# Kernel tuning notes

Measured on AMD Instinct MI355X. Metric: run time of the kernel, lower is better.

The kernel has to match this reference:

```python
import jax, jax.numpy as jnp
import numpy as np

HEADS = 4
DIM_HEAD = 64


def setup_inputs() -> dict:
    key = jax.random.key(0)
    k1, k2, k3, k4 = jax.random.split(key, 4)
    dim = 256
    hidden = HEADS * DIM_HEAD  # 256
    x = jax.random.normal(k1, (16, dim, 64, 64), dtype=jnp.float32)
    # 1x1 conv weights stored as [out_c, in_c]
    w_qkv = jax.random.normal(k2, (3 * hidden, dim), dtype=jnp.float32) * (1.0 / np.sqrt(dim))
    w_out = jax.random.normal(k3, (dim, hidden), dtype=jnp.float32) * (1.0 / np.sqrt(hidden))
    b_out = jax.random.normal(k4, (dim,), dtype=jnp.float32) * 0.01
    gamma = jnp.ones((dim,), dtype=jnp.float32) * 1e-05
    return {"x": x, "w_qkv": w_qkv, "w_out": w_out, "b_out": b_out, "gamma": gamma}


def reference(x, w_qkv, w_out, b_out, gamma):
    b, c, h, w = x.shape
    n = h * w
    # 1x1 conv == channel matmul
    qkv = jnp.einsum('oc,bchw->bohw', w_qkv, x)  # [b, 3*heads*dh, h, w]
    qkv = qkv.reshape(b, 3, HEADS, DIM_HEAD, n)  # channel split order: (qkv, heads, c)
    q, k, v = qkv[:, 0], qkv[:, 1], qkv[:, 2]    # each [b, heads, dh, n]
    k = jax.nn.softmax(k, axis=-1)               # softmax over spatial tokens
    context = jnp.einsum('bhdn,bhen->bhde', k, v)  # [b, heads, dh, dh]
    out = jnp.einsum('bhde,bhdn->bhen', context, q)  # [b, heads, dh, n]
    out = out.reshape(b, HEADS * DIM_HEAD, h, w)
    y = jnp.einsum('oc,bchw->bohw', w_out, out) + b_out[None, :, None, None]
    return y * gamma[None, :, None, None] + x
```

## Files before the change

### kernel.cpp

```cpp
#include <hip/hip_runtime.h>
#include <stdint.h>

typedef short s16x8 __attribute__((ext_vector_type(8)));
typedef float f32x4 __attribute__((ext_vector_type(4)));

__device__ __forceinline__ float bits2f(unsigned short u) {
    union { unsigned int i; float f; } c; c.i = ((unsigned int)u) << 16; return c.f;
}
__device__ __forceinline__ unsigned short f2bits(float f) {
    union { float f; unsigned int i; } c; c.f = f;
    unsigned int x = c.i;
    unsigned int r = (x + 0x7FFFu + ((x >> 16) & 1u)) >> 16;
    return (unsigned short)r;
}
__device__ __forceinline__ unsigned int pack2(float a, float b) {
    return (unsigned int)f2bits(a) | ((unsigned int)f2bits(b) << 16);
}

__global__ __launch_bounds__(256) void k_cvt(
    const float* __restrict__ src, unsigned short* __restrict__ dst, int n8)
{
    int i = blockIdx.x * 256 + threadIdx.x;
    if (i >= n8) return;
    const float* s = src + (size_t)i * 8;
    float4 a = *(const float4*)s, b = *(const float4*)(s + 4);
    unsigned int q[4] = { pack2(a.x, a.y), pack2(a.z, a.w), pack2(b.x, b.y), pack2(b.z, b.w) };
    *(s16x8*)(dst + (size_t)i * 8) = *(s16x8*)q;
}

__global__ __launch_bounds__(256) void k_transpose(
    const unsigned short* __restrict__ src, unsigned short* __restrict__ dst,
    int RS, int DS)
{
    int dr = blockIdx.x * 256 + threadIdx.x;
    int c0 = blockIdx.y * 8;
    __align__(16) unsigned short tmp[8];
#pragma unroll
    for (int j = 0; j < 8; ++j) tmp[j] = src[(size_t)(c0 + j) * RS + dr];
    *(s16x8*)(dst + (size_t)dr * DS + c0) = *(s16x8*)tmp;
}

template <int BF32>
__global__ __launch_bounds__(256) void gemm_bt(
    const unsigned short* __restrict__ A, const void* __restrict__ Bt,
    unsigned short* __restrict__ C,
    int K, int Kstep, int lda, int ldb, int ldc,
    long Abs, long Bbs, long Cbs)
{
    __shared__ unsigned short As[128][72];
    __shared__ unsigned short Bs[128][72];
    int bz = blockIdx.z;
    int b = bz & 15, kc = bz >> 4;
    int m0 = blockIdx.y * 128, n0 = blockIdx.x * 128;
    const unsigned short* Ab = A + (size_t)b * Abs + (size_t)m0 * lda + (size_t)kc * Kstep;
    size_t boff = (size_t)b * Bbs + (size_t)n0 * ldb + (size_t)kc * Kstep;
    int t = threadIdx.x;
    int w = t >> 6, l = t & 63, lm = l & 15, lq = l >> 4;
    int mw = (w >> 1) * 64, nw = (w & 1) * 64;

    f32x4 acc[4][4];
    f32x4 zero = {0.f, 0.f, 0.f, 0.f};
#pragma unroll
    for (int i = 0; i < 4; ++i)
#pragma unroll
        for (int j = 0; j < 4; ++j) acc[i][j] = zero;

    for (int kk = 0; kk < K; kk += 64) {
#pragma unroll
        for (int i = 0; i < 4; ++i) {
            int idx = t + i * 256;
            int r = idx >> 3, ch = idx & 7;
            *(s16x8*)&As[r][ch * 8] = *(const s16x8*)(Ab + (size_t)r * lda + kk + ch * 8);
            if (BF32) {
                const float* bp = (const float*)Bt + boff + (size_t)r * ldb + kk + ch * 8;
                float4 v0 = *(const float4*)bp, v1 = *(const float4*)(bp + 4);
                unsigned int q[4] = { pack2(v0.x, v0.y), pack2(v0.z, v0.w),
                                      pack2(v1.x, v1.y), pack2(v1.z, v1.w) };
                *(s16x8*)&Bs[r][ch * 8] = *(s16x8*)q;
            } else {
                const unsigned short* bp = (const unsigned short*)Bt + boff + (size_t)r * ldb + kk + ch * 8;
                *(s16x8*)&Bs[r][ch * 8] = *(const s16x8*)bp;
            }
        }
        __syncthreads();
#pragma unroll
        for (int ks = 0; ks < 2; ++ks) {
            s16x8 af[4], bfr[4];
#pragma unroll
            for (int mi = 0; mi < 4; ++mi) af[mi]  = *(const s16x8*)&As[mw + mi * 16 + lm][ks * 32 + lq * 8];
#pragma unroll
            for (int ni = 0; ni < 4; ++ni) bfr[ni] = *(const s16x8*)&Bs[nw + ni * 16 + lm][ks * 32 + lq * 8];
#pragma unroll
            for (int mi = 0; mi < 4; ++mi)
#pragma unroll
                for (int ni = 0; ni < 4; ++ni)
                    acc[mi][ni] = __builtin_amdgcn_mfma_f32_16x16x32_bf16(af[mi], bfr[ni], acc[mi][ni], 0, 0, 0);
        }
        __syncthreads();
    }

    unsigned short* Cb = C + (size_t)bz * Cbs;
#pragma unroll
    for (int mi = 0; mi < 4; ++mi)
#pragma unroll
        for (int r = 0; r < 4; ++r) {
            int m = m0 + mw + mi * 16 + lq * 4 + r;
#pragma unroll
            for (int ni = 0; ni < 4; ++ni) {
                int n = n0 + nw + ni * 16 + lm;
                Cb[(size_t)m * ldc + n] = f2bits(acc[mi][ni][r]);
            }
        }
}

template <int EPI>
__global__ __launch_bounds__(256) void gemm_bn(
    const unsigned short* __restrict__ A, const float* __restrict__ B,
    void* __restrict__ C,
    int K, int lda, int ldb, int ldc,
    long Abs, long Bbs, long Cbs,
    const float* __restrict__ Xres,
    const float* __restrict__ gamma,
    const float* __restrict__ bias)
{
    __shared__ unsigned short As[128][72];
    __shared__ unsigned short Bs[64][130];
    int bz = blockIdx.z;
    int m0 = blockIdx.y * 128, n0 = blockIdx.x * 128;
    const unsigned short* Ab = A + (size_t)bz * Abs + (size_t)m0 * lda;
    const float* Bb = B + (size_t)bz * Bbs + n0;
    int t = threadIdx.x;
    int w = t >> 6, l = t & 63, lm = l & 15, lq = l >> 4;
    int mw = (w >> 1) * 64, nw = (w & 1) * 64;

    f32x4 acc[4][4];
    f32x4 zero = {0.f, 0.f, 0.f, 0.f};
#pragma unroll
    for (int i = 0; i < 4; ++i)
#pragma unroll
        for (int j = 0; j < 4; ++j) acc[i][j] = zero;

    for (int kk = 0; kk < K; kk += 64) {
#pragma unroll
        for (int i = 0; i < 4; ++i) {
            int idx = t + i * 256;
            int r = idx >> 3, ch = idx & 7;
            *(s16x8*)&As[r][ch * 8] = *(const s16x8*)(Ab + (size_t)r * lda + kk + ch * 8);
        }
#pragma unroll
        for (int i = 0; i < 4; ++i) {
            int idx = t + i * 256;
            int c = idx >> 4, cc = idx & 15;
            const float* bp = Bb + (size_t)(kk + c) * ldb + cc * 8;
            float4 v0 = *(const float4*)bp, v1 = *(const float4*)(bp + 4);
            unsigned int* q = (unsigned int*)&Bs[c][cc * 8];
            q[0] = pack2(v0.x, v0.y); q[1] = pack2(v0.z, v0.w);
            q[2] = pack2(v1.x, v1.y); q[3] = pack2(v1.z, v1.w);
        }
        __syncthreads();
#pragma unroll
        for (int ks = 0; ks < 2; ++ks) {
            s16x8 af[4];
#pragma unroll
            for (int mi = 0; mi < 4; ++mi) af[mi] = *(const s16x8*)&As[mw + mi * 16 + lm][ks * 32 + lq * 8];
#pragma unroll
            for (int ni = 0; ni < 4; ++ni) {
                s16x8 bfr;
#pragma unroll
                for (int j = 0; j < 8; ++j) bfr[j] = (short)Bs[ks * 32 + lq * 8 + j][nw + ni * 16 + lm];
#pragma unroll
                for (int mi = 0; mi < 4; ++mi)
                    acc[mi][ni] = __builtin_amdgcn_mfma_f32_16x16x32_bf16(af[mi], bfr, acc[mi][ni], 0, 0, 0);
            }
        }
        __syncthreads();
    }

#pragma unroll
    for (int mi = 0; mi < 4; ++mi)
#pragma unroll
        for (int r = 0; r < 4; ++r) {
            int m = m0 + mw + mi * 16 + lq * 4 + r;
            float g = 0.f, bo = 0.f;
            if (EPI == 1) { g = gamma[m]; bo = bias[m]; }
#pragma unroll
            for (int ni = 0; ni < 4; ++ni) {
                int n = n0 + nw + ni * 16 + lm;
                size_t idx = (size_t)m * ldc + n;
                float v = acc[mi][ni][r];
                if (EPI == 1) {
                    float* Cb = (float*)C + (size_t)bz * Cbs;
                    Cb[idx] = g * (v + bo) + Xres[(size_t)bz * Cbs + idx];
                } else {
                    unsigned short* Cb = (unsigned short*)C + (size_t)bz * Cbs;
                    Cb[idx] = f2bits(v);
                }
            }
        }
}

__global__ __launch_bounds__(256) void k_softmax(unsigned short* __restrict__ kbuf)
{
    unsigned short* p = kbuf + (size_t)blockIdx.x * 4096;
    int t = threadIdx.x;
    __shared__ float red[4];

    s16x8 r0 = *(const s16x8*)(p + t * 16);
    s16x8 r1 = *(const s16x8*)(p + t * 16 + 8);
    float v[16];
    float m = -1e30f;
#pragma unroll
    for (int i = 0; i < 8; ++i) { v[i] = bits2f((unsigned short)r0[i]); v[8 + i] = bits2f((unsigned short)r1[i]); }
#pragma unroll
    for (int i = 0; i < 16; ++i) m = fmaxf(m, v[i]);
#pragma unroll
    for (int off = 32; off >= 1; off >>= 1) m = fmaxf(m, __shfl_xor(m, off));
    if ((t & 63) == 0) red[t >> 6] = m;
    __syncthreads();
    m = fmaxf(fmaxf(red[0], red[1]), fmaxf(red[2], red[3]));
    __syncthreads();

    float s = 0.f;
#pragma unroll
    for (int i = 0; i < 16; ++i) { v[i] = __expf(v[i] - m); s += v[i]; }
#pragma unroll
    for (int off = 32; off >= 1; off >>= 1) s += __shfl_xor(s, off);
    if ((t & 63) == 0) red[t >> 6] = s;
    __syncthreads();
    s = red[0] + red[1] + red[2] + red[3];
    float inv = 1.0f / s;

    __align__(16) unsigned short otmp[16];
#pragma unroll
    for (int i = 0; i < 16; ++i) otmp[i] = f2bits(v[i] * inv);
    *(s16x8*)(p + t * 16) = *(s16x8*)(otmp);
    *(s16x8*)(p + t * 16 + 8) = *(s16x8*)(otmp + 8);
}

__global__ __launch_bounds__(256) void k_gred(
    const unsigned short* __restrict__ Gp, unsigned short* __restrict__ G)
{
    int gid = blockIdx.x * 256 + threadIdx.x;
    int b = gid >> 13;
    size_t i8 = (size_t)(gid & 8191) * 8;
    float s[8] = {0.f, 0.f, 0.f, 0.f, 0.f, 0.f, 0.f, 0.f};
#pragma unroll
    for (int kc = 0; kc < 8; ++kc) {
        s16x8 v = *(const s16x8*)(Gp + (size_t)(kc * 16 + b) * 65536 + i8);
#pragma unroll
        for (int j = 0; j < 8; ++j) s[j] += bits2f((unsigned short)v[j]);
    }
    __align__(16) unsigned short tmp[8];
#pragma unroll
    for (int j = 0; j < 8; ++j) tmp[j] = f2bits(s[j]);
    *(s16x8*)(G + (size_t)b * 65536 + i8) = *(s16x8*)tmp;
}

__global__ __launch_bounds__(256) void k_ctxw2(
    const unsigned short* __restrict__ G, const unsigned short* __restrict__ wb,
    const unsigned short* __restrict__ wob, unsigned short* __restrict__ W2)
{
    __shared__ unsigned short ctxs[64][72];
    int h = blockIdx.x, b = blockIdx.y;
    int t = threadIdx.x, w = t >> 6, l = t & 63, lm = l & 15, lq = l >> 4;
    const unsigned short* Gb = G + (size_t)b * 65536 + (size_t)(h * 64) * 256;
    const unsigned short* Wv = wb + 131072 + (size_t)(h * 64) * 256;
    f32x4 zero = {0.f, 0.f, 0.f, 0.f};

    f32x4 acc[4];
#pragma unroll
    for (int i = 0; i < 4; ++i) acc[i] = zero;
    for (int kk = 0; kk < 256; kk += 32) {
        s16x8 a = *(const s16x8*)(Gb + (size_t)(w * 16 + lm) * 256 + kk + lq * 8);
#pragma unroll
        for (int ni = 0; ni < 4; ++ni) {
            s16x8 bb = *(const s16x8*)(Wv + (size_t)(ni * 16 + lm) * 256 + kk + lq * 8);
            acc[ni] = __builtin_amdgcn_mfma_f32_16x16x32_bf16(a, bb, acc[ni], 0, 0, 0);
        }
    }
#pragma unroll
    for (int ni = 0; ni < 4; ++ni)
#pragma unroll
        for (int r = 0; r < 4; ++r)
            ctxs[w * 16 + lq * 4 + r][ni * 16 + lm] = f2bits(acc[ni][r]);
    __syncthreads();

    f32x4 acc2[4][4];
#pragma unroll
    for (int i = 0; i < 4; ++i)
#pragma unroll
        for (int j = 0; j < 4; ++j) acc2[i][j] = zero;
#pragma unroll
    for (int ks = 0; ks < 2; ++ks) {
        s16x8 af[4], bfr[4];
#pragma unroll
        for (int mi = 0; mi < 4; ++mi)
            af[mi] = *(const s16x8*)(wob + (size_t)(w * 64 + mi * 16 + lm) * 256 + h * 64 + ks * 32 + lq * 8);
#pragma unroll
        for (int ni = 0; ni < 4; ++ni) bfr[ni] = *(const s16x8*)&ctxs[ni * 16 + lm][ks * 32 + lq * 8];
#pragma unroll
        for (int mi = 0; mi < 4; ++mi)
#pragma unroll
            for (int ni = 0; ni < 4; ++ni)
                acc2[mi][ni] = __builtin_amdgcn_mfma_f32_16x16x32_bf16(af[mi], bfr[ni], acc2[mi][ni], 0, 0, 0);
    }
    unsigned short* W2b = W2 + (size_t)b * 65536;
#pragma unroll
    for (int mi = 0; mi < 4; ++mi)
#pragma unroll
        for (int r = 0; r < 4; ++r) {
            int o = w * 64 + mi * 16 + lq * 4 + r;
#pragma unroll
            for (int ni = 0; ni < 4; ++ni)
                W2b[(size_t)o * 256 + h * 64 + ni * 16 + lm] = f2bits(acc2[mi][ni][r]);
        }
}

extern "C" void kernel_launch(void* const* d_in, const int* in_sizes, int n_in,
                              void* d_out, int out_size, void* d_ws, size_t ws_size,
                              hipStream_t stream)
{
    (void)in_sizes; (void)n_in; (void)out_size; (void)ws_size;
    const float* x      = (const float*)d_in[0];
    const float* w_qkv  = (const float*)d_in[1];
    const float* w_out  = (const float*)d_in[2];
    const float* b_out  = (const float*)d_in[3];
    const float* gamma  = (const float*)d_in[4];
    unsigned short* kbuf = (unsigned short*)d_out;

    char* ws = (char*)d_ws;
    unsigned short* Gp  = (unsigned short*)(ws);
    unsigned short* G   = (unsigned short*)(ws + 16777216);
    unsigned short* W2  = (unsigned short*)(ws + 18874368);
    unsigned short* W3  = (unsigned short*)(ws + 20971520);
    unsigned short* WqT = (unsigned short*)(ws + 23068672);
    unsigned short* wb  = (unsigned short*)(ws + 23199744);
    unsigned short* wob = (unsigned short*)(ws + 23592960);

    k_cvt<<<dim3(96), 256, 0, stream>>>(w_qkv, wb, 24576);
    k_cvt<<<dim3(32), 256, 0, stream>>>(w_out, wob, 8192);

    k_transpose<<<dim3(1, 32, 1), 256, 0, stream>>>(wb, WqT, 256, 256);

    gemm_bn<0><<<dim3(32, 2, 16), 256, 0, stream>>>(
        wb + 65536, x, kbuf, 256, 256, 4096, 4096,
        0L, 1048576L, 1048576L, nullptr, nullptr, nullptr);

    k_softmax<<<dim3(4096), 256, 0, stream>>>(kbuf);

    gemm_bt<1><<<dim3(2, 2, 128), 256, 0, stream>>>(
        kbuf, x, Gp, 512, 512, 4096, 4096, 256,
        1048576L, 1048576L, 65536L);

    k_gred<<<dim3(512), 256, 0, stream>>>(Gp, G);

    k_ctxw2<<<dim3(4, 16), 256, 0, stream>>>(G, wb, wob, W2);

    gemm_bt<0><<<dim3(2, 2, 16), 256, 0, stream>>>(
        W2, WqT, W3, 256, 0, 256, 256, 256,
        65536L, 0L, 65536L);

    gemm_bn<1><<<dim3(32, 2, 16), 256, 0, stream>>>(
        W3, x, d_out, 256, 256, 4096, 4096,
        65536L, 1048576L, 1048576L, x, gamma, b_out);
}
```

Baseline: 229.3 us.

## Fuse softmax normalization into context GEMM and cache bf16 x copy

The K projection GEMM now also writes a bf16 copy of x, which later GEMMs read instead of converting fp32 x again. The softmax kernel only computes per-row max and inverse sum, and the exponentiation and normalization move into the A-tile load of the context GEMM. The separate partial-sum reduction kernel is removed by having k_ctxw2 loop over the eight K-chunks itself. A new wide-M GEMM (256x64 tiles) replaces the 128x128 version for the projection and output stages. The aim is fewer launches and less full-size memory traffic, at the cost of an extra 32MB bf16 write and bf16-rounded x in the output GEMM's B operand.

```diff
diff --git a/kernel.cpp b/kernel.cpp
--- a/kernel.cpp
+++ b/kernel.cpp
@@ -40,10 +40,107 @@
     *(s16x8*)(dst + (size_t)dr * DS + c0) = *(s16x8*)tmp;
 }
 
-template <int BF32>
+template <int EPI, int BBF16, int XCVT>
+__global__ __launch_bounds__(256) void gemm_wide(
+    const unsigned short* __restrict__ A, const void* __restrict__ B,
+    void* __restrict__ C, unsigned short* __restrict__ xbout,
+    const float* __restrict__ Xres, const float* __restrict__ gamma,
+    const float* __restrict__ bias, long Abs)
+{
+    __shared__ unsigned short As[256][72];
+    __shared__ unsigned short Bs[64][66];
+    int bz = blockIdx.z;
+    int n0 = blockIdx.x * 64;
+    const unsigned short* Ab = A + (size_t)bz * Abs;
+    int t = threadIdx.x, w = t >> 6, l = t & 63, lm = l & 15, lq = l >> 4;
+    int mw = w * 64;
+
+    f32x4 acc[4][4];
+    f32x4 zero = {0.f, 0.f, 0.f, 0.f};
+#pragma unroll
+    for (int i = 0; i < 4; ++i)
+#pragma unroll
+        for (int j = 0; j < 4; ++j) acc[i][j] = zero;
+
+    for (int kk = 0; kk < 256; kk += 64) {
+#pragma unroll
+        for (int i = 0; i < 8; ++i) {
+            int idx = t + i * 256;
+            int r = idx >> 3, ch = idx & 7;
+            *(s16x8*)&As[r][ch * 8] = *(const s16x8*)(Ab + (size_t)r * 256 + kk + ch * 8);
+        }
+#pragma unroll
+        for (int i = 0; i < 2; ++i) {
+            int idx = t + i * 256;
+            int c = idx >> 3, ch = idx & 7;
+            unsigned int* qp = (unsigned int*)&Bs[c][ch * 8];
+            if (BBF16) {
+                const unsigned short* bp = (const unsigned short*)B + (size_t)bz * 1048576
+                                         + (size_t)(kk + c) * 4096 + n0 + ch * 8;
+                union { s16x8 v; unsigned int u[4]; } cv;
+                cv.v = *(const s16x8*)bp;
+                qp[0] = cv.u[0]; qp[1] = cv.u[1]; qp[2] = cv.u[2]; qp[3] = cv.u[3];
+            } else {
+                const float* bp = (const float*)B + (size_t)bz * 1048576
+                                + (size_t)(kk + c) * 4096 + n0 + ch * 8;
+                float4 v0 = *(const float4*)bp, v1 = *(const float4*)(bp + 4);
+                unsigned int q[4] = { pack2(v0.x, v0.y), pack2(v0.z, v0.w),
+                                      pack2(v1.x, v1.y), pack2(v1.z, v1.w) };
+                qp[0] = q[0]; qp[1] = q[1]; qp[2] = q[2]; qp[3] = q[3];
+                if (XCVT) {
+                    unsigned short* xp = xbout + (size_t)bz * 1048576
+                                       + (size_t)(kk + c) * 4096 + n0 + ch * 8;
+                    *(s16x8*)xp = *(s16x8*)q;
+                }
+            }
+        }
+        __syncthreads();
+#pragma unroll
+        for (int ks = 0; ks < 2; ++ks) {
+            s16x8 af[4];
+#pragma unroll
+            for (int mi = 0; mi < 4; ++mi)
+                af[mi] = *(const s16x8*)&As[mw + mi * 16 + lm][ks * 32 + lq * 8];
+#pragma unroll
+            for (int ni = 0; ni < 4; ++ni) {
+                s16x8 bfr;
+#pragma unroll
+                for (int j = 0; j < 8; ++j) bfr[j] = (short)Bs[ks * 32 + lq * 8 + j][ni * 16 + lm];
+#pragma unroll
+                for (int mi = 0; mi < 4; ++mi)
+                    acc[mi][ni] = __builtin_amdgcn_mfma_f32_16x16x32_bf16(af[mi], bfr, acc[mi][ni], 0, 0, 0);
+            }
+        }
+        __syncthreads();
+    }
+
+#pragma unroll
+    for (int mi = 0; mi < 4; ++mi)
+#pragma unroll
+        for (int r = 0; r < 4; ++r) {
+            int m = mw + mi * 16 + lq * 4 + r;
+            float g = 0.f, bo = 0.f;
+            if (EPI == 1) { g = gamma[m]; bo = bias[m]; }
+#pragma unroll
+            for (int ni = 0; ni < 4; ++ni) {
+                int n = n0 + ni * 16 + lm;
+                size_t idx = (size_t)m * 4096 + n;
+                float v = acc[mi][ni][r];
+                if (EPI == 1) {
+                    float* Cb = (float*)C + (size_t)bz * 1048576;
+                    Cb[idx] = g * (v + bo) + Xres[(size_t)bz * 1048576 + idx];
+                } else {
+                    unsigned short* Cb = (unsigned short*)C + (size_t)bz * 1048576;
+                    Cb[idx] = f2bits(v);
+                }
+            }
+        }
+}
+
+template <int AEXP>
 __global__ __launch_bounds__(256) void gemm_bt(
-    const unsigned short* __restrict__ A, const void* __restrict__ Bt,
-    unsigned short* __restrict__ C,
+    const unsigned short* __restrict__ A, const unsigned short* __restrict__ Bt,
+    unsigned short* __restrict__ C, const float2* __restrict__ stats,
     int K, int Kstep, int lda, int ldb, int ldc,
     long Abs, long Bbs, long Cbs)
 {
@@ -53,7 +150,7 @@
     int b = bz & 15, kc = bz >> 4;
     int m0 = blockIdx.y * 128, n0 = blockIdx.x * 128;
     const unsigned short* Ab = A + (size_t)b * Abs + (size_t)m0 * lda + (size_t)kc * Kstep;
-    size_t boff = (size_t)b * Bbs + (size_t)n0 * ldb + (size_t)kc * Kstep;
+    const unsigned short* Bb = Bt + (size_t)b * Bbs + (size_t)n0 * ldb + (size_t)kc * Kstep;
     int t = threadIdx.x;
     int w = t >> 6, l = t & 63, lm = l & 15, lq = l >> 4;
     int mw = (w >> 1) * 64, nw = (w & 1) * 64;
@@ -70,17 +167,20 @@
         for (int i = 0; i < 4; ++i) {
             int idx = t + i * 256;
             int r = idx >> 3, ch = idx & 7;
-            *(s16x8*)&As[r][ch * 8] = *(const s16x8*)(Ab + (size_t)r * lda + kk + ch * 8);
-            if (BF32) {
-                const float* bp = (const float*)Bt + boff + (size_t)r * ldb + kk + ch * 8;
-                float4 v0 = *(const float4*)bp, v1 = *(const float4*)(bp + 4);
-                unsigned int q[4] = { pack2(v0.x, v0.y), pack2(v0.z, v0.w),
-                                      pack2(v1.x, v1.y), pack2(v1.z, v1.w) };
-                *(s16x8*)&Bs[r][ch * 8] = *(s16x8*)q;
-            } else {
-                const unsigned short* bp = (const unsigned short*)Bt + boff + (size_t)r * ldb + kk + ch * 8;
-                *(s16x8*)&Bs[r][ch * 8] = *(const s16x8*)bp;
-            }
+            s16x8 av = *(const s16x8*)(Ab + (size_t)r * lda + kk + ch * 8);
+            if (AEXP) {
+                float2 st = stats[b * 256 + m0 + r];
+                unsigned int q[4];
+#pragma unroll
+                for (int j = 0; j < 4; ++j) {
+                    float e0 = __expf(bits2f((unsigned short)av[2 * j]) - st.x) * st.y;
+                    float e1 = __expf(bits2f((unsigned short)av[2 * j + 1]) - st.x) * st.y;
+                    q[j] = pack2(e0, e1);
+                }
+                av = *(s16x8*)q;
+            }
+            *(s16x8*)&As[r][ch * 8] = av;
+            *(s16x8*)&Bs[r][ch * 8] = *(const s16x8*)(Bb + (size_t)r * ldb + kk + ch * 8);
         }
         __syncthreads();
 #pragma unroll
@@ -113,95 +213,10 @@
         }
 }
 
-template <int EPI>
-__global__ __launch_bounds__(256) void gemm_bn(
-    const unsigned short* __restrict__ A, const float* __restrict__ B,
-    void* __restrict__ C,
-    int K, int lda, int ldb, int ldc,
-    long Abs, long Bbs, long Cbs,
-    const float* __restrict__ Xres,
-    const float* __restrict__ gamma,
-    const float* __restrict__ bias)
-{
-    __shared__ unsigned short As[128][72];
-    __shared__ unsigned short Bs[64][130];
-    int bz = blockIdx.z;
-    int m0 = blockIdx.y * 128, n0 = blockIdx.x * 128;
-    const unsigned short* Ab = A + (size_t)bz * Abs + (size_t)m0 * lda;
-    const float* Bb = B + (size_t)bz * Bbs + n0;
-    int t = threadIdx.x;
-    int w = t >> 6, l = t & 63, lm = l & 15, lq = l >> 4;
-    int mw = (w >> 1) * 64, nw = (w & 1) * 64;
-
-    f32x4 acc[4][4];
-    f32x4 zero = {0.f, 0.f, 0.f, 0.f};
-#pragma unroll
-    for (int i = 0; i < 4; ++i)
-#pragma unroll
-        for (int j = 0; j < 4; ++j) acc[i][j] = zero;
-
-    for (int kk = 0; kk < K; kk += 64) {
-#pragma unroll
-        for (int i = 0; i < 4; ++i) {
-            int idx = t + i * 256;
-            int r = idx >> 3, ch = idx & 7;
-            *(s16x8*)&As[r][ch * 8] = *(const s16x8*)(Ab + (size_t)r * lda + kk + ch * 8);
-        }
-#pragma unroll
-        for (int i = 0; i < 4; ++i) {
-            int idx = t + i * 256;
-            int c = idx >> 4, cc = idx & 15;
-            const float* bp = Bb + (size_t)(kk + c) * ldb + cc * 8;
-            float4 v0 = *(const float4*)bp, v1 = *(const float4*)(bp + 4);
-            unsigned int* q = (unsigned int*)&Bs[c][cc * 8];
-            q[0] = pack2(v0.x, v0.y); q[1] = pack2(v0.z, v0.w);
-            q[2] = pack2(v1.x, v1.y); q[3] = pack2(v1.z, v1.w);
-        }
-        __syncthreads();
-#pragma unroll
-        for (int ks = 0; ks < 2; ++ks) {
-            s16x8 af[4];
-#pragma unroll
-            for (int mi = 0; mi < 4; ++mi) af[mi] = *(const s16x8*)&As[mw + mi * 16 + lm][ks * 32 + lq * 8];
-#pragma unroll
-            for (int ni = 0; ni < 4; ++ni) {
-                s16x8 bfr;
-#pragma unroll
-                for (int j = 0; j < 8; ++j) bfr[j] = (short)Bs[ks * 32 + lq * 8 + j][nw + ni * 16 + lm];
-#pragma unroll
-                for (int mi = 0; mi < 4; ++mi)
-                    acc[mi][ni] = __builtin_amdgcn_mfma_f32_16x16x32_bf16(af[mi], bfr, acc[mi][ni], 0, 0, 0);
-            }
-        }
-        __syncthreads();
-    }
-
-#pragma unroll
-    for (int mi = 0; mi < 4; ++mi)
-#pragma unroll
-        for (int r = 0; r < 4; ++r) {
-            int m = m0 + mw + mi * 16 + lq * 4 + r;
-            float g = 0.f, bo = 0.f;
-            if (EPI == 1) { g = gamma[m]; bo = bias[m]; }
-#pragma unroll
-            for (int ni = 0; ni < 4; ++ni) {
-                int n = n0 + nw + ni * 16 + lm;
-                size_t idx = (size_t)m * ldc + n;
-                float v = acc[mi][ni][r];
-                if (EPI == 1) {
-                    float* Cb = (float*)C + (size_t)bz * Cbs;
-                    Cb[idx] = g * (v + bo) + Xres[(size_t)bz * Cbs + idx];
-                } else {
-                    unsigned short* Cb = (unsigned short*)C + (size_t)bz * Cbs;
-                    Cb[idx] = f2bits(v);
-                }
-            }
-        }
-}
-
-__global__ __launch_bounds__(256) void k_softmax(unsigned short* __restrict__ kbuf)
-{
-    unsigned short* p = kbuf + (size_t)blockIdx.x * 4096;
+__global__ __launch_bounds__(256) void k_softstats(
+    const unsigned short* __restrict__ kbuf, float2* __restrict__ stats)
+{
+    const unsigned short* p = kbuf + (size_t)blockIdx.x * 4096;
     int t = threadIdx.x;
     __shared__ float red[4];
 
@@ -222,60 +237,40 @@
 
     float s = 0.f;
 #pragma unroll
-    for (int i = 0; i < 16; ++i) { v[i] = __expf(v[i] - m); s += v[i]; }
+    for (int i = 0; i < 16; ++i) s += __expf(v[i] - m);
 #pragma unroll
     for (int off = 32; off >= 1; off >>= 1) s += __shfl_xor(s, off);
     if ((t & 63) == 0) red[t >> 6] = s;
     __syncthreads();
-    s = red[0] + red[1] + red[2] + red[3];
-    float inv = 1.0f / s;
-
-    __align__(16) unsigned short otmp[16];
-#pragma unroll
-    for (int i = 0; i < 16; ++i) otmp[i] = f2bits(v[i] * inv);
-    *(s16x8*)(p + t * 16) = *(s16x8*)(otmp);
-    *(s16x8*)(p + t * 16 + 8) = *(s16x8*)(otmp + 8);
-}
-
-__global__ __launch_bounds__(256) void k_gred(
-    const unsigned short* __restrict__ Gp, unsigned short* __restrict__ G)
-{
-    int gid = blockIdx.x * 256 + threadIdx.x;
-    int b = gid >> 13;
-    size_t i8 = (size_t)(gid & 8191) * 8;
-    float s[8] = {0.f, 0.f, 0.f, 0.f, 0.f, 0.f, 0.f, 0.f};
-#pragma unroll
-    for (int kc = 0; kc < 8; ++kc) {
-        s16x8 v = *(const s16x8*)(Gp + (size_t)(kc * 16 + b) * 65536 + i8);
-#pragma unroll
-        for (int j = 0; j < 8; ++j) s[j] += bits2f((unsigned short)v[j]);
-    }
-    __align__(16) unsigned short tmp[8];
-#pragma unroll
-    for (int j = 0; j < 8; ++j) tmp[j] = f2bits(s[j]);
-    *(s16x8*)(G + (size_t)b * 65536 + i8) = *(s16x8*)tmp;
+    if (t == 0) {
+        s = red[0] + red[1] + red[2] + red[3];
+        stats[blockIdx.x] = make_float2(m, 1.0f / s);
+    }
 }
 
 __global__ __launch_bounds__(256) void k_ctxw2(
-    const unsigned short* __restrict__ G, const unsigned short* __restrict__ wb,
+    const unsigned short* __restrict__ Gp, const unsigned short* __restrict__ wb,
     const unsigned short* __restrict__ wob, unsigned short* __restrict__ W2)
 {
     __shared__ unsigned short ctxs[64][72];
     int h = blockIdx.x, b = blockIdx.y;
     int t = threadIdx.x, w = t >> 6, l = t & 63, lm = l & 15, lq = l >> 4;
-    const unsigned short* Gb = G + (size_t)b * 65536 + (size_t)(h * 64) * 256;
     const unsigned short* Wv = wb + 131072 + (size_t)(h * 64) * 256;
     f32x4 zero = {0.f, 0.f, 0.f, 0.f};
 
     f32x4 acc[4];
 #pragma unroll
     for (int i = 0; i < 4; ++i) acc[i] = zero;
-    for (int kk = 0; kk < 256; kk += 32) {
-        s16x8 a = *(const s16x8*)(Gb + (size_t)(w * 16 + lm) * 256 + kk + lq * 8);
-#pragma unroll
-        for (int ni = 0; ni < 4; ++ni) {
-            s16x8 bb = *(const s16x8*)(Wv + (size_t)(ni * 16 + lm) * 256 + kk + lq * 8);
-            acc[ni] = __builtin_amdgcn_mfma_f32_16x16x32_bf16(a, bb, acc[ni], 0, 0, 0);
+    for (int kc = 0; kc < 8; ++kc) {
+        const unsigned short* Gb = Gp + (size_t)(kc * 16 + b) * 65536 + (size_t)(h * 64) * 256;
+#pragma unroll
+        for (int kk = 0; kk < 256; kk += 32) {
+            s16x8 a = *(const s16x8*)(Gb + (size_t)(w * 16 + lm) * 256 + kk + lq * 8);
+#pragma unroll
+            for (int ni = 0; ni < 4; ++ni) {
+                s16x8 bb = *(const s16x8*)(Wv + (size_t)(ni * 16 + lm) * 256 + kk + lq * 8);
+                acc[ni] = __builtin_amdgcn_mfma_f32_16x16x32_bf16(a, bb, acc[ni], 0, 0, 0);
+            }
         }
     }
 #pragma unroll
@@ -329,38 +324,34 @@
     unsigned short* kbuf = (unsigned short*)d_out;
 
     char* ws = (char*)d_ws;
-    unsigned short* Gp  = (unsigned short*)(ws);
-    unsigned short* G   = (unsigned short*)(ws + 16777216);
-    unsigned short* W2  = (unsigned short*)(ws + 18874368);
-    unsigned short* W3  = (unsigned short*)(ws + 20971520);
-    unsigned short* WqT = (unsigned short*)(ws + 23068672);
-    unsigned short* wb  = (unsigned short*)(ws + 23199744);
-    unsigned short* wob = (unsigned short*)(ws + 23592960);
+    unsigned short* xb  = (unsigned short*)(ws);
+    unsigned short* Gp  = (unsigned short*)(ws + 33554432);
+    unsigned short* W2  = (unsigned short*)(ws + 50331648);
+    unsigned short* W3  = (unsigned short*)(ws + 52428800);
+    unsigned short* WqT = (unsigned short*)(ws + 54525952);
+    unsigned short* wb  = (unsigned short*)(ws + 54657024);
+    unsigned short* wob = (unsigned short*)(ws + 55050240);
+    float2*         st  = (float2*)        (ws + 55181312);
 
     k_cvt<<<dim3(96), 256, 0, stream>>>(w_qkv, wb, 24576);
     k_cvt<<<dim3(32), 256, 0, stream>>>(w_out, wob, 8192);
-
     k_transpose<<<dim3(1, 32, 1), 256, 0, stream>>>(wb, WqT, 256, 256);
 
-    gemm_bn<0><<<dim3(32, 2, 16), 256, 0, stream>>>(
-        wb + 65536, x, kbuf, 256, 256, 4096, 4096,
-        0L, 1048576L, 1048576L, nullptr, nullptr, nullptr);
-
-    k_softmax<<<dim3(4096), 256, 0, stream>>>(kbuf);
+    gemm_wide<0, 0, 1><<<dim3(64, 1, 16), 256, 0, stream>>>(
+        wb + 65536, x, kbuf, xb, nullptr, nullptr, nullptr, 0L);
+
+    k_softstats<<<dim3(4096), 256, 0, stream>>>(kbuf, st);
 
     gemm_bt<1><<<dim3(2, 2, 128), 256, 0, stream>>>(
-        kbuf, x, Gp, 512, 512, 4096, 4096, 256,
+        kbuf, xb, Gp, st, 512, 512, 4096, 4096, 256,
         1048576L, 1048576L, 65536L);
 
-    k_gred<<<dim3(512), 256, 0, stream>>>(Gp, G);
-
-    k_ctxw2<<<dim3(4, 16), 256, 0, stream>>>(G, wb, wob, W2);
+    k_ctxw2<<<dim3(4, 16), 256, 0, stream>>>(Gp, wb, wob, W2);
 
     gemm_bt<0><<<dim3(2, 2, 16), 256, 0, stream>>>(
-        W2, WqT, W3, 256, 0, 256, 256, 256,
+        W2, WqT, W3, nullptr, 256, 0, 256, 256, 256,
         65536L, 0L, 65536L);
 
-    gemm_bn<1><<<dim3(32, 2, 16), 256, 0, stream>>>(
-        W3, x, d_out, 256, 256, 4096, 4096,
-        65536L, 1048576L, 1048576L, x, gamma, b_out);
-}
+    gemm_wide<1, 1, 0><<<dim3(64, 1, 16), 256, 0, stream>>>(
+        W3, xb, d_out, nullptr, x, gamma, b_out, 65536L);
+}
```

Result: slower. 239.9 us (+4.6%).
